# Optimization experiments

Hardware: AMD Instinct MI355X
Metric: run time of the kernel (lower is better)

## Reference

```python
import jax, jax.numpy as jnp
import numpy as np

T, B, E, H = 2048, 2, 1024, 16
HD = E // H
L, R = 8, 4
SCALE = HD ** -0.5
NEG = -1e9


def setup_inputs() -> dict:
    key = jax.random.key(0)
    ks = jax.random.split(key, 14)
    c = 0.5  # sqrt(1/rank) constant init for multiplicative factors (fast=True)
    inp = {
        'hidden_states': jax.random.normal(ks[0], (T, B, E), jnp.float32),
        'proj_weight': jax.random.normal(ks[1], (3 * E, E), jnp.float32) * (E ** -0.5),
        'proj_bias': jax.random.normal(ks[2], (3 * E,), jnp.float32) * 0.02,
        'out_weight': jax.random.normal(ks[3], (E, E), jnp.float32) * (E ** -0.5),
        'out_bias': jax.random.normal(ks[4], (E,), jnp.float32) * 0.02,
        'rm_i': c + 0.01 * jax.random.normal(ks[5], (L, R, 3 * E), jnp.float32),
        'sm_i': c + 0.01 * jax.random.normal(ks[6], (L, R, E), jnp.float32),
        'rm_o': c + 0.01 * jax.random.normal(ks[7], (L, R, E), jnp.float32),
        'sm_o': c + 0.01 * jax.random.normal(ks[8], (L, R, E), jnp.float32),
        'r_i': 0.01 * jax.random.normal(ks[9], (L, R, 3 * E), jnp.float32),
        's_i': 0.01 * jax.random.normal(ks[10], (L, R, E), jnp.float32),
        'r_o': 0.01 * jax.random.normal(ks[11], (L, R, E), jnp.float32),
        's_o': 0.01 * jax.random.normal(ks[12], (L, R, E), jnp.float32),
        'lang': jax.random.randint(ks[13], (1,), 0, L, jnp.int32),
    }
    return inp


def reference(hidden_states, proj_weight, proj_bias, out_weight, out_bias,
              rm_i, sm_i, rm_o, sm_o, r_i, s_i, r_o, s_o, lang):
    li = lang[0]
    # multiplicative low-rank modulation (fast_factorize: mm of rank-R factors)
    mul_in = jnp.einsum('re,rf->ef', rm_i[li], sm_i[li])   # [3E, E]
    mul_out = jnp.einsum('re,rf->ef', rm_o[li], sm_o[li])  # [E, E]
    add_in = jnp.einsum('re,rf->ef', r_i[li], s_i[li])
    add_out = jnp.einsum('re,rf->ef', r_o[li], s_o[li])
    w_in = proj_weight * mul_in + add_in    # [3E, E]
    w_out = out_weight * mul_out + add_out  # [E, E]

    # fused QKV projection; rows of w_in are laid out as [H, 3, HD]
    qkv = hidden_states @ w_in.T + proj_bias            # [T, B, 3E]
    qkv = qkv.reshape(T, B, H, 3, HD)
    q = qkv[..., 0, :] * SCALE                          # [T, B, H, HD]
    k = qkv[..., 1, :]
    v = qkv[..., 2, :]

    scores = jnp.einsum('tbhd,sbhd->bhts', q, k)        # [B, H, T, T]
    causal = jnp.tril(jnp.ones((T, T), bool))           # time mask (is_decoder)
    scores = jnp.where(causal, scores, NEG)
    attn = jax.nn.softmax(scores, axis=-1)
    ctx = jnp.einsum('bhts,sbhd->tbhd', attn, v).reshape(T, B, E)
    out = ctx @ w_out.T + out_bias                      # [T, B, E]
    return out
```

## Files before the change

kernel.cpp:

```cpp
#include <hip/hip_runtime.h>
#include <hip/hip_bf16.h>

typedef __attribute__((ext_vector_type(8))) short short8;
typedef __attribute__((ext_vector_type(4))) float f32x4;
typedef unsigned short u16;

#define NEGINF (-1e9f)

__device__ __forceinline__ u16 f2bf(float x) {
    union { float f; unsigned int u; } v; v.f = x;
    unsigned int r = v.u + 0x7fff + ((v.u >> 16) & 1);
    return (u16)(r >> 16);
}

__device__ __forceinline__ float fast_exp2(float x) {
    float r;
    asm volatile("v_exp_f32 %0, %1" : "=v"(r) : "v"(x));
    return r;
}

__device__ __forceinline__ void gload16(const void* g, void* l) {
    __builtin_amdgcn_global_load_lds(
        (const __attribute__((address_space(1))) unsigned int*)g,
        (__attribute__((address_space(3))) unsigned int*)l, 16, 0, 0);
}

__global__ __launch_bounds__(256) void cast_hidden_kernel(const float* __restrict__ in,
                                                          u16* __restrict__ out) {
    int idx = (blockIdx.x * 256 + threadIdx.x) * 4;
    float4 v = *(const float4*)&in[idx];
    ushort4 o;
    o.x = f2bf(v.x); o.y = f2bf(v.y); o.z = f2bf(v.z); o.w = f2bf(v.w);
    *(ushort4*)&out[idx] = o;
}

__global__ __launch_bounds__(256) void prep_w_kernel(const float* __restrict__ w,
                                                     const float* __restrict__ rm,
                                                     const float* __restrict__ sm,
                                                     const float* __restrict__ ra,
                                                     const float* __restrict__ sa,
                                                     const int* __restrict__ lang,
                                                     u16* __restrict__ out, int rows) {
    const int li = lang[0];
    int idx = blockIdx.x * 256 + threadIdx.x;
    int e = idx >> 8;
    int f = (idx & 255) * 4;
    float4 pw = *(const float4*)&w[(size_t)e * 1024 + f];
    float mul0 = 0.f, mul1 = 0.f, mul2 = 0.f, mul3 = 0.f;
    float add0 = 0.f, add1 = 0.f, add2 = 0.f, add3 = 0.f;
#pragma unroll
    for (int r = 0; r < 4; r++) {
        float a = rm[(size_t)(li * 4 + r) * rows + e];
        float4 b = *(const float4*)&sm[(size_t)(li * 4 + r) * 1024 + f];
        float c = ra[(size_t)(li * 4 + r) * rows + e];
        float4 d = *(const float4*)&sa[(size_t)(li * 4 + r) * 1024 + f];
        mul0 += a * b.x; mul1 += a * b.y; mul2 += a * b.z; mul3 += a * b.w;
        add0 += c * d.x; add1 += c * d.y; add2 += c * d.z; add3 += c * d.w;
    }
    ushort4 o;
    o.x = f2bf(pw.x * mul0 + add0);
    o.y = f2bf(pw.y * mul1 + add1);
    o.z = f2bf(pw.z * mul2 + add2);
    o.w = f2bf(pw.w * mul3 + add3);
    *(ushort4*)&out[(size_t)e * 1024 + f] = o;
}

template <int EPI>
__global__ __launch_bounds__(256) void gemm_bf16(const u16* __restrict__ A,
                                                 const u16* __restrict__ W,
                                                 const float* __restrict__ bias,
                                                 int K,
                                                 float* __restrict__ outF,
                                                 u16* __restrict__ qb,
                                                 u16* __restrict__ kb,
                                                 u16* __restrict__ vb) {
    __shared__ __align__(16) u16 As[128 * 32];
    __shared__ __align__(16) u16 Bs[128 * 32];
    const int t = threadIdx.x;
    const int lane = t & 63, wv = t >> 6;
    const int lr = lane & 15, lk = lane >> 4;
    const int wr = wv >> 1, wc = wv & 1;
    const int m0 = blockIdx.y * 128, n0 = blockIdx.x * 128;

    const int rowS = t >> 2, kcS = t & 3;
    const u16* gA0 = A + (size_t)(m0 + rowS) * K + kcS * 8;
    const u16* gA1 = gA0 + (size_t)64 * K;
    const u16* gB0 = W + (size_t)(n0 + rowS) * K + kcS * 8;
    const u16* gB1 = gB0 + (size_t)64 * K;
    char* ldsA0 = (char*)As + wv * 1024;
    char* ldsA1 = (char*)As + 4096 + wv * 1024;
    char* ldsB0 = (char*)Bs + wv * 1024;
    char* ldsB1 = (char*)Bs + 4096 + wv * 1024;

    f32x4 acc[4][4] = {};

    for (int k0 = 0; k0 < K; k0 += 32) {
        gload16(gA0 + k0, ldsA0);
        gload16(gA1 + k0, ldsA1);
        gload16(gB0 + k0, ldsB0);
        gload16(gB1 + k0, ldsB1);
        __syncthreads();
        short8 af[4], bf[4];
#pragma unroll
        for (int mi = 0; mi < 4; mi++)
            af[mi] = *(const short8*)&As[(wr * 64 + mi * 16 + lr) * 32 + lk * 8];
#pragma unroll
        for (int ni = 0; ni < 4; ni++)
            bf[ni] = *(const short8*)&Bs[(wc * 64 + ni * 16 + lr) * 32 + lk * 8];
#pragma unroll
        for (int mi = 0; mi < 4; mi++)
#pragma unroll
            for (int ni = 0; ni < 4; ni++)
                acc[mi][ni] = __builtin_amdgcn_mfma_f32_16x16x32_bf16(af[mi], bf[ni], acc[mi][ni], 0, 0, 0);
        __syncthreads();
    }

#pragma unroll
    for (int mi = 0; mi < 4; mi++) {
#pragma unroll
        for (int ni = 0; ni < 4; ni++) {
            int n = n0 + wc * 64 + ni * 16 + lr;
            float bv = bias[n];
#pragma unroll
            for (int i = 0; i < 4; i++) {
                int m = m0 + wr * 64 + mi * 16 + lk * 4 + i;
                float val = acc[mi][ni][i] + bv;
                if (EPI == 0) {
                    int tt = m >> 1, bb = m & 1;
                    int h = n / 192;
                    int rem = n - h * 192;
                    int s = rem >> 6, d = rem & 63;
                    size_t bh = (size_t)(bb * 16 + h);
                    if (s == 0)      qb[(bh * 2048 + tt) * 64 + d] = f2bf(val * 0.18033688f);
                    else if (s == 1) kb[(bh * 2048 + tt) * 64 + d] = f2bf(val);
                    else             vb[(bh * 2048 + tt) * 64 + d] = f2bf(val);
                } else {
                    outF[(size_t)m * 1024 + n] = val;
                }
            }
        }
    }
}

__global__ __launch_bounds__(256) void tr_v_kernel(const u16* __restrict__ vb,
                                                   u16* __restrict__ vtb) {
    __shared__ u16 tile[64][72];
    const int bh = blockIdx.y;
    const int t0 = blockIdx.x * 64;
    const int tid = threadIdx.x;
    const int row = tid >> 3, c8 = (tid & 7) * 8;
#pragma unroll
    for (int p = 0; p < 2; p++) {
        short8 v = *(const short8*)&vb[((size_t)bh * 2048 + t0 + row + p * 32) * 64 + c8];
        *(short8*)&tile[row + p * 32][c8] = v;
    }
    __syncthreads();
    const int d = tid >> 2, tg = (tid & 3) * 16;
    short8 a, b;
#pragma unroll
    for (int j = 0; j < 8; j++) a[j] = tile[tg + j][d];
#pragma unroll
    for (int j = 0; j < 8; j++) b[j] = tile[tg + 8 + j][d];
    *(short8*)&vtb[((size_t)bh * 64 + d) * 2048 + t0 + tg] = a;
    *(short8*)&vtb[((size_t)bh * 64 + d) * 2048 + t0 + tg + 8] = b;
}

__global__ __launch_bounds__(256) void attn_kernel(const u16* __restrict__ qb,
                                                   const u16* __restrict__ kb,
                                                   const u16* __restrict__ vtb,
                                                   u16* __restrict__ ctx) {
    __shared__ __align__(16) u16 Ks[2][4096];
    __shared__ __align__(16) u16 Vs[2][4096];
    __shared__ __align__(16) u16 Plds[4][16][72];

    const int t = threadIdx.x;
    const int lane = t & 63, wv = t >> 6;
    const int lr = lane & 15, lk = lane >> 4;

    const int d = blockIdx.x;
    const int bh = (d & 7) * 4 + ((d >> 3) >> 4);
    const int pair = (d >> 3) & 15;

    const u16* Kg = kb + (size_t)bh * 2048 * 64;
    const u16* Vg = vtb + (size_t)bh * 64 * 2048;
    const int bb = bh >> 4, h = bh & 15;

    const int p0 = wv * 64 + lane;
    const int r0 = p0 >> 3, c0 = (p0 & 7) ^ (r0 & 7);
    const int p1 = 256 + p0;
    const int r1 = p1 >> 3, c1 = (p1 & 7) ^ (r1 & 7);
    const int ldsOff0 = (wv * 64) * 8;
    const int ldsOff1 = (256 + wv * 64) * 8;

#pragma unroll 1
    for (int sidx = 0; sidx < 2; sidx++) {
        const int strip = sidx == 0 ? pair : 31 - pair;
        const int q0 = strip * 64 + wv * 16;
        const u16* Qp = qb + ((size_t)bh * 2048 + q0) * 64;
        short8 qf0 = *(const short8*)&Qp[lr * 64 + lk * 8];
        short8 qf1 = *(const short8*)&Qp[lr * 64 + 32 + lk * 8];

        f32x4 acc[4] = {};
        float mrow = -3e38f, ssum = 0.f;

        const int nt = strip + 1;
        int buf = 0;

        {
            gload16(Kg + (size_t)(0 + r0) * 64 + c0 * 8, &Ks[0][ldsOff0]);
            gload16(Kg + (size_t)(0 + r1) * 64 + c1 * 8, &Ks[0][ldsOff1]);
            gload16(Vg + (size_t)r0 * 2048 + 0 + c0 * 8, &Vs[0][ldsOff0]);
            gload16(Vg + (size_t)r1 * 2048 + 0 + c1 * 8, &Vs[0][ldsOff1]);
        }
        asm volatile("s_waitcnt vmcnt(0)" ::: "memory");
        __syncthreads();

#pragma unroll 1
        for (int tt = 0; tt < nt; tt++) {
            const int kv0 = tt * 64;
            if (tt + 1 < nt) {
                const int nkv = kv0 + 64;
                gload16(Kg + (size_t)(nkv + r0) * 64 + c0 * 8, &Ks[buf ^ 1][ldsOff0]);
                gload16(Kg + (size_t)(nkv + r1) * 64 + c1 * 8, &Ks[buf ^ 1][ldsOff1]);
                gload16(Vg + (size_t)r0 * 2048 + nkv + c0 * 8, &Vs[buf ^ 1][ldsOff0]);
                gload16(Vg + (size_t)r1 * 2048 + nkv + c1 * 8, &Vs[buf ^ 1][ldsOff1]);
            }

            f32x4 sb[4];
#pragma unroll
            for (int nj = 0; nj < 4; nj++) {
                const int r = nj * 16 + lr;
                short8 kf0 = *(const short8*)&Ks[buf][r * 64 + ((lk    ) ^ (r & 7)) * 8];
                short8 kf1 = *(const short8*)&Ks[buf][r * 64 + ((lk + 4) ^ (r & 7)) * 8];
                f32x4 z = {0.f, 0.f, 0.f, 0.f};
                z = __builtin_amdgcn_mfma_f32_16x16x32_bf16(kf0, qf0, z, 0, 0, 0);
                z = __builtin_amdgcn_mfma_f32_16x16x32_bf16(kf1, qf1, z, 0, 0, 0);
                sb[nj] = z;
            }
            if (kv0 + 63 > q0) {
                const int qr = q0 + lr;
#pragma unroll
                for (int nj = 0; nj < 4; nj++) {
                    const int kvb = kv0 + nj * 16 + lk * 4;
#pragma unroll
                    for (int i = 0; i < 4; i++)
                        if (kvb + i > qr) sb[nj][i] = NEGINF;
                }
            }

            float pm0 = fmaxf(fmaxf(sb[0][0], sb[0][1]), fmaxf(sb[0][2], sb[0][3]));
            float pm1 = fmaxf(fmaxf(sb[1][0], sb[1][1]), fmaxf(sb[1][2], sb[1][3]));
            float pm2 = fmaxf(fmaxf(sb[2][0], sb[2][1]), fmaxf(sb[2][2], sb[2][3]));
            float pm3 = fmaxf(fmaxf(sb[3][0], sb[3][1]), fmaxf(sb[3][2], sb[3][3]));
            float pmax = fmaxf(fmaxf(pm0, pm1), fmaxf(pm2, pm3));
            pmax = fmaxf(pmax, __shfl_xor(pmax, 16));
            pmax = fmaxf(pmax, __shfl_xor(pmax, 32));
            const float mold = mrow;
            const float mnew = fmaxf(mold, pmax);
            const float scl = fast_exp2(mold - mnew);
            mrow = mnew;
            float psum = 0.f;
#pragma unroll
            for (int nj = 0; nj < 4; nj++)
#pragma unroll
                for (int i = 0; i < 4; i++) {
                    float p = fast_exp2(sb[nj][i] - mnew);
                    sb[nj][i] = p;
                    psum += p;
                }
            psum += __shfl_xor(psum, 16);
            psum += __shfl_xor(psum, 32);
            ssum = ssum * scl + psum;

#pragma unroll
            for (int nj = 0; nj < 4; nj++) {
                ushort4 pk4;
                pk4.x = f2bf(sb[nj][0]); pk4.y = f2bf(sb[nj][1]);
                pk4.z = f2bf(sb[nj][2]); pk4.w = f2bf(sb[nj][3]);
                *(ushort4*)&Plds[wv][lr][nj * 16 + lk * 4] = pk4;
            }

            if (!__all(pmax <= mold)) {
                float s0 = __shfl(scl, lk * 4 + 0);
                float s1 = __shfl(scl, lk * 4 + 1);
                float s2 = __shfl(scl, lk * 4 + 2);
                float s3 = __shfl(scl, lk * 4 + 3);
#pragma unroll
                for (int ni = 0; ni < 4; ni++) {
                    acc[ni][0] *= s0; acc[ni][1] *= s1;
                    acc[ni][2] *= s2; acc[ni][3] *= s3;
                }
            }

            short8 pf0 = *(const short8*)&Plds[wv][lr][lk * 8];
            short8 pf1 = *(const short8*)&Plds[wv][lr][32 + lk * 8];
#pragma unroll
            for (int ni = 0; ni < 4; ni++) {
                const int r = ni * 16 + lr;
                short8 vf0 = *(const short8*)&Vs[buf][r * 64 + ((lk    ) ^ (r & 7)) * 8];
                short8 vf1 = *(const short8*)&Vs[buf][r * 64 + ((lk + 4) ^ (r & 7)) * 8];
                acc[ni] = __builtin_amdgcn_mfma_f32_16x16x32_bf16(pf0, vf0, acc[ni], 0, 0, 0);
                acc[ni] = __builtin_amdgcn_mfma_f32_16x16x32_bf16(pf1, vf1, acc[ni], 0, 0, 0);
            }

            asm volatile("s_waitcnt vmcnt(0)" ::: "memory");
            __syncthreads();
            buf ^= 1;
        }

        float rs0 = 1.0f / __shfl(ssum, lk * 4 + 0);
        float rs1 = 1.0f / __shfl(ssum, lk * 4 + 1);
        float rs2 = 1.0f / __shfl(ssum, lk * 4 + 2);
        float rs3 = 1.0f / __shfl(ssum, lk * 4 + 3);
#pragma unroll
        for (int ni = 0; ni < 4; ni++) {
            int tq = q0 + lk * 4;
            int col = h * 64 + ni * 16 + lr;
            ctx[(size_t)((tq + 0) * 2 + bb) * 1024 + col] = f2bf(acc[ni][0] * rs0);
            ctx[(size_t)((tq + 1) * 2 + bb) * 1024 + col] = f2bf(acc[ni][1] * rs1);
            ctx[(size_t)((tq + 2) * 2 + bb) * 1024 + col] = f2bf(acc[ni][2] * rs2);
            ctx[(size_t)((tq + 3) * 2 + bb) * 1024 + col] = f2bf(acc[ni][3] * rs3);
        }
        __syncthreads();
    }
}

extern "C" void kernel_launch(void* const* d_in, const int* in_sizes, int n_in,
                              void* d_out, int out_size, void* d_ws, size_t ws_size,
                              hipStream_t stream) {
    const float* hs     = (const float*)d_in[0];
    const float* proj_w = (const float*)d_in[1];
    const float* proj_b = (const float*)d_in[2];
    const float* out_w  = (const float*)d_in[3];
    const float* out_b  = (const float*)d_in[4];
    const float* rm_i   = (const float*)d_in[5];
    const float* sm_i   = (const float*)d_in[6];
    const float* rm_o   = (const float*)d_in[7];
    const float* sm_o   = (const float*)d_in[8];
    const float* r_i    = (const float*)d_in[9];
    const float* s_i    = (const float*)d_in[10];
    const float* r_o    = (const float*)d_in[11];
    const float* s_o    = (const float*)d_in[12];
    const int*   lang   = (const int*)d_in[13];
    float* out = (float*)d_out;

    char* ws = (char*)d_ws;
    u16* hsb   = (u16*)(ws);
    u16* w_in  = (u16*)(ws + (size_t)(8 << 20));
    u16* w_out = (u16*)(ws + (size_t)(14 << 20));
    u16* qb    = (u16*)(ws + (size_t)(16 << 20));
    u16* kb    = (u16*)(ws + (size_t)(24 << 20));
    u16* vtb   = (u16*)(ws + (size_t)(32 << 20));
    u16* ctxb  = (u16*)(ws + (size_t)(40 << 20));
    u16* vb    = ctxb;

    cast_hidden_kernel<<<dim3(4096), dim3(256), 0, stream>>>(hs, hsb);
    prep_w_kernel<<<dim3(3072), dim3(256), 0, stream>>>(proj_w, rm_i, sm_i, r_i, s_i, lang, w_in, 3072);
    prep_w_kernel<<<dim3(1024), dim3(256), 0, stream>>>(out_w, rm_o, sm_o, r_o, s_o, lang, w_out, 1024);
    gemm_bf16<0><<<dim3(24, 32), dim3(256), 0, stream>>>(hsb, w_in, proj_b, 1024, (float*)nullptr, qb, kb, vb);
    tr_v_kernel<<<dim3(32, 32), dim3(256), 0, stream>>>(vb, vtb);
    attn_kernel<<<dim3(512), dim3(256), 0, stream>>>(qb, kb, vtb, ctxb);
    gemm_bf16<1><<<dim3(8, 32), dim3(256), 0, stream>>>(ctxb, w_out, out_b, 1024, out, (u16*)nullptr, (u16*)nullptr, (u16*)nullptr);
}
```

Before: 234.7 us.

## Keep softmax P in registers via lane shuffles and narrow output GEMM tiles

In the attention kernel, the P matrix is no longer written to and read back from shared memory. It is packed to bf16 with v_cvt_pk_bf16 and rearranged into the MFMA A-operand layout using cross-lane xor shuffles, which removes the LDS round trip and a buffer. Separately, the output projection GEMM gets its own kernel with 128x64 tiles, doubling the grid to 512 blocks so more CUs are busy. The costs are extra shuffle instructions in the inner loop and less reuse per tile in the output GEMM.

```diff
diff --git a/kernel.cpp b/kernel.cpp
--- a/kernel.cpp
+++ b/kernel.cpp
@@ -4,6 +4,7 @@
 typedef __attribute__((ext_vector_type(8))) short short8;
 typedef __attribute__((ext_vector_type(4))) float f32x4;
 typedef unsigned short u16;
+typedef unsigned int u32;
 
 #define NEGINF (-1e9f)
 
@@ -16,6 +17,12 @@
 __device__ __forceinline__ float fast_exp2(float x) {
     float r;
     asm volatile("v_exp_f32 %0, %1" : "=v"(r) : "v"(x));
+    return r;
+}
+
+__device__ __forceinline__ u32 cvt_pk_bf16(float a, float b) {
+    u32 r;
+    asm("v_cvt_pk_bf16_f32 %0, %1, %2" : "=v"(r) : "v"(a), "v"(b));
     return r;
 }
 
@@ -65,15 +72,13 @@
     *(ushort4*)&out[(size_t)e * 1024 + f] = o;
 }
 
-template <int EPI>
-__global__ __launch_bounds__(256) void gemm_bf16(const u16* __restrict__ A,
-                                                 const u16* __restrict__ W,
-                                                 const float* __restrict__ bias,
-                                                 int K,
-                                                 float* __restrict__ outF,
-                                                 u16* __restrict__ qb,
-                                                 u16* __restrict__ kb,
-                                                 u16* __restrict__ vb) {
+__global__ __launch_bounds__(256) void gemm_qkv(const u16* __restrict__ A,
+                                                const u16* __restrict__ W,
+                                                const float* __restrict__ bias,
+                                                int K,
+                                                u16* __restrict__ qb,
+                                                u16* __restrict__ kb,
+                                                u16* __restrict__ vb) {
     __shared__ __align__(16) u16 As[128 * 32];
     __shared__ __align__(16) u16 Bs[128 * 32];
     const int t = threadIdx.x;
@@ -125,18 +130,72 @@
             for (int i = 0; i < 4; i++) {
                 int m = m0 + wr * 64 + mi * 16 + lk * 4 + i;
                 float val = acc[mi][ni][i] + bv;
-                if (EPI == 0) {
-                    int tt = m >> 1, bb = m & 1;
-                    int h = n / 192;
-                    int rem = n - h * 192;
-                    int s = rem >> 6, d = rem & 63;
-                    size_t bh = (size_t)(bb * 16 + h);
-                    if (s == 0)      qb[(bh * 2048 + tt) * 64 + d] = f2bf(val * 0.18033688f);
-                    else if (s == 1) kb[(bh * 2048 + tt) * 64 + d] = f2bf(val);
-                    else             vb[(bh * 2048 + tt) * 64 + d] = f2bf(val);
-                } else {
-                    outF[(size_t)m * 1024 + n] = val;
-                }
+                int tt = m >> 1, bb = m & 1;
+                int h = n / 192;
+                int rem = n - h * 192;
+                int s = rem >> 6, d = rem & 63;
+                size_t bh = (size_t)(bb * 16 + h);
+                if (s == 0)      qb[(bh * 2048 + tt) * 64 + d] = f2bf(val * 0.18033688f);
+                else if (s == 1) kb[(bh * 2048 + tt) * 64 + d] = f2bf(val);
+                else             vb[(bh * 2048 + tt) * 64 + d] = f2bf(val);
+            }
+        }
+    }
+}
+
+__global__ __launch_bounds__(256) void gemm_out(const u16* __restrict__ A,
+                                                const u16* __restrict__ W,
+                                                const float* __restrict__ bias,
+                                                float* __restrict__ outF) {
+    __shared__ __align__(16) u16 As[128 * 32];
+    __shared__ __align__(16) u16 Bs[64 * 32];
+    const int K = 1024;
+    const int t = threadIdx.x;
+    const int lane = t & 63, wv = t >> 6;
+    const int lr = lane & 15, lk = lane >> 4;
+    const int wr = wv >> 1, wc = wv & 1;
+    const int m0 = blockIdx.y * 128, n0 = blockIdx.x * 64;
+
+    const int rowS = t >> 2, kcS = t & 3;
+    const u16* gA0 = A + (size_t)(m0 + rowS) * K + kcS * 8;
+    const u16* gA1 = gA0 + (size_t)64 * K;
+    const u16* gB0 = W + (size_t)(n0 + rowS) * K + kcS * 8;
+    char* ldsA0 = (char*)As + wv * 1024;
+    char* ldsA1 = (char*)As + 4096 + wv * 1024;
+    char* ldsB0 = (char*)Bs + wv * 1024;
+
+    f32x4 acc[4][2] = {};
+
+    for (int k0 = 0; k0 < K; k0 += 32) {
+        gload16(gA0 + k0, ldsA0);
+        gload16(gA1 + k0, ldsA1);
+        gload16(gB0 + k0, ldsB0);
+        __syncthreads();
+        short8 af[4], bf[2];
+#pragma unroll
+        for (int mi = 0; mi < 4; mi++)
+            af[mi] = *(const short8*)&As[(wr * 64 + mi * 16 + lr) * 32 + lk * 8];
+#pragma unroll
+        for (int ni = 0; ni < 2; ni++)
+            bf[ni] = *(const short8*)&Bs[(wc * 32 + ni * 16 + lr) * 32 + lk * 8];
+#pragma unroll
+        for (int mi = 0; mi < 4; mi++)
+#pragma unroll
+            for (int ni = 0; ni < 2; ni++)
+                acc[mi][ni] = __builtin_amdgcn_mfma_f32_16x16x32_bf16(af[mi], bf[ni], acc[mi][ni], 0, 0, 0);
+        __syncthreads();
+    }
+
+#pragma unroll
+    for (int mi = 0; mi < 4; mi++) {
+#pragma unroll
+        for (int ni = 0; ni < 2; ni++) {
+            int n = n0 + wc * 32 + ni * 16 + lr;
+            float bv = bias[n];
+#pragma unroll
+            for (int i = 0; i < 4; i++) {
+                int m = m0 + wr * 64 + mi * 16 + lk * 4 + i;
+                outF[(size_t)m * 1024 + n] = acc[mi][ni][i] + bv;
             }
         }
     }
@@ -171,11 +230,11 @@
                                                    u16* __restrict__ ctx) {
     __shared__ __align__(16) u16 Ks[2][4096];
     __shared__ __align__(16) u16 Vs[2][4096];
-    __shared__ __align__(16) u16 Plds[4][16][72];
 
     const int t = threadIdx.x;
     const int lane = t & 63, wv = t >> 6;
     const int lr = lane & 15, lk = lane >> 4;
+    const int b4 = lk & 1, bx = (lk & 1) ^ (lk >> 1);
 
     const int d = blockIdx.x;
     const int bh = (d & 7) * 4 + ((d >> 3) >> 4);
@@ -272,35 +331,53 @@
             psum += __shfl_xor(psum, 32);
             ssum = ssum * scl + psum;
 
-#pragma unroll
-            for (int nj = 0; nj < 4; nj++) {
-                ushort4 pk4;
-                pk4.x = f2bf(sb[nj][0]); pk4.y = f2bf(sb[nj][1]);
-                pk4.z = f2bf(sb[nj][2]); pk4.w = f2bf(sb[nj][3]);
-                *(ushort4*)&Plds[wv][lr][nj * 16 + lk * 4] = pk4;
-            }
+            u32 e00 = cvt_pk_bf16(sb[0][0], sb[0][1]);
+            u32 e01 = cvt_pk_bf16(sb[0][2], sb[0][3]);
+            u32 e10 = cvt_pk_bf16(sb[1][0], sb[1][1]);
+            u32 e11 = cvt_pk_bf16(sb[1][2], sb[1][3]);
+            u32 e20 = cvt_pk_bf16(sb[2][0], sb[2][1]);
+            u32 e21 = cvt_pk_bf16(sb[2][2], sb[2][3]);
+            u32 e30 = cvt_pk_bf16(sb[3][0], sb[3][1]);
+            u32 e31 = cvt_pk_bf16(sb[3][2], sb[3][3]);
+            u32 s0 = b4 ? e00 : e10, s1 = b4 ? e01 : e11;
+            u32 s2 = b4 ? e20 : e30, s3 = b4 ? e21 : e31;
+            u32 ra0 = __shfl_xor((int)s0, 16), ra1 = __shfl_xor((int)s1, 16);
+            u32 ra2 = __shfl_xor((int)s2, 16), ra3 = __shfl_xor((int)s3, 16);
+            u32 kA0 = b4 ? e10 : e00, kA1 = b4 ? e11 : e01;
+            u32 kA2 = b4 ? e30 : e20, kA3 = b4 ? e31 : e21;
+            u32 g0 = b4 ? ra0 : kA0, g1 = b4 ? ra1 : kA1;
+            u32 g2 = b4 ? kA0 : ra0, g3 = b4 ? kA1 : ra1;
+            u32 g4 = b4 ? ra2 : kA2, g5 = b4 ? ra3 : kA3;
+            u32 g6 = b4 ? kA2 : ra2, g7 = b4 ? kA3 : ra3;
+            u32 h0 = __shfl_xor((int)g0, 48), h1 = __shfl_xor((int)g1, 48);
+            u32 h2 = __shfl_xor((int)g2, 48), h3 = __shfl_xor((int)g3, 48);
+            u32 h4 = __shfl_xor((int)g4, 48), h5 = __shfl_xor((int)g5, 48);
+            u32 h6 = __shfl_xor((int)g6, 48), h7 = __shfl_xor((int)g7, 48);
+            union { u32 u[4]; short8 s; } P0, P1;
+            P0.u[0] = bx ? h0 : g0; P0.u[1] = bx ? h1 : g1;
+            P0.u[2] = bx ? h2 : g2; P0.u[3] = bx ? h3 : g3;
+            P1.u[0] = bx ? h4 : g4; P1.u[1] = bx ? h5 : g5;
+            P1.u[2] = bx ? h6 : g6; P1.u[3] = bx ? h7 : g7;
 
             if (!__all(pmax <= mold)) {
-                float s0 = __shfl(scl, lk * 4 + 0);
-                float s1 = __shfl(scl, lk * 4 + 1);
-                float s2 = __shfl(scl, lk * 4 + 2);
-                float s3 = __shfl(scl, lk * 4 + 3);
+                float t0s = __shfl(scl, lk * 4 + 0);
+                float t1s = __shfl(scl, lk * 4 + 1);
+                float t2s = __shfl(scl, lk * 4 + 2);
+                float t3s = __shfl(scl, lk * 4 + 3);
 #pragma unroll
                 for (int ni = 0; ni < 4; ni++) {
-                    acc[ni][0] *= s0; acc[ni][1] *= s1;
-                    acc[ni][2] *= s2; acc[ni][3] *= s3;
+                    acc[ni][0] *= t0s; acc[ni][1] *= t1s;
+                    acc[ni][2] *= t2s; acc[ni][3] *= t3s;
                 }
             }
 
-            short8 pf0 = *(const short8*)&Plds[wv][lr][lk * 8];
-            short8 pf1 = *(const short8*)&Plds[wv][lr][32 + lk * 8];
 #pragma unroll
             for (int ni = 0; ni < 4; ni++) {
                 const int r = ni * 16 + lr;
                 short8 vf0 = *(const short8*)&Vs[buf][r * 64 + ((lk    ) ^ (r & 7)) * 8];
                 short8 vf1 = *(const short8*)&Vs[buf][r * 64 + ((lk + 4) ^ (r & 7)) * 8];
-                acc[ni] = __builtin_amdgcn_mfma_f32_16x16x32_bf16(pf0, vf0, acc[ni], 0, 0, 0);
-                acc[ni] = __builtin_amdgcn_mfma_f32_16x16x32_bf16(pf1, vf1, acc[ni], 0, 0, 0);
+                acc[ni] = __builtin_amdgcn_mfma_f32_16x16x32_bf16(P0.s, vf0, acc[ni], 0, 0, 0);
+                acc[ni] = __builtin_amdgcn_mfma_f32_16x16x32_bf16(P1.s, vf1, acc[ni], 0, 0, 0);
             }
 
             asm volatile("s_waitcnt vmcnt(0)" ::: "memory");
@@ -357,8 +434,8 @@
     cast_hidden_kernel<<<dim3(4096), dim3(256), 0, stream>>>(hs, hsb);
     prep_w_kernel<<<dim3(3072), dim3(256), 0, stream>>>(proj_w, rm_i, sm_i, r_i, s_i, lang, w_in, 3072);
     prep_w_kernel<<<dim3(1024), dim3(256), 0, stream>>>(out_w, rm_o, sm_o, r_o, s_o, lang, w_out, 1024);
-    gemm_bf16<0><<<dim3(24, 32), dim3(256), 0, stream>>>(hsb, w_in, proj_b, 1024, (float*)nullptr, qb, kb, vb);
+    gemm_qkv<<<dim3(24, 32), dim3(256), 0, stream>>>(hsb, w_in, proj_b, 1024, qb, kb, vb);
     tr_v_kernel<<<dim3(32, 32), dim3(256), 0, stream>>>(vb, vtb);
     attn_kernel<<<dim3(512), dim3(256), 0, stream>>>(qb, kb, vtb, ctxb);
-    gemm_bf16<1><<<dim3(8, 32), dim3(256), 0, stream>>>(ctxb, w_out, out_b, 1024, out, (u16*)nullptr, (u16*)nullptr, (u16*)nullptr);
-}
+    gemm_out<<<dim3(16, 32), dim3(256), 0, stream>>>(ctxb, w_out, out_b, out);
+}
```

Measured after the change: 229.4 us. 1.02x faster.
